# Optimization experiments

Measured on AMD Instinct MI355X. Metric: run time of the kernel, lower is better.

Reference implementation:

```python
import jax, jax.numpy as jnp
import numpy as np

D_MODEL = 1024
D_HEAD = 128


def setup_inputs() -> dict:
    key = jax.random.key(0)
    kx, kq, kk, kv, ko = jax.random.split(key, 5)
    x = jax.random.normal(kx, (4, 2048, D_MODEL), dtype=jnp.float32)
    # xavier-uniform-ish init scale
    s_in = (6.0 / (D_MODEL + D_HEAD)) ** 0.5
    wq = jax.random.uniform(kq, (D_MODEL, D_HEAD), minval=-s_in, maxval=s_in, dtype=jnp.float32)
    wk = jax.random.uniform(kk, (D_MODEL, D_HEAD), minval=-s_in, maxval=s_in, dtype=jnp.float32)
    wv = jax.random.uniform(kv, (D_MODEL, D_HEAD), minval=-s_in, maxval=s_in, dtype=jnp.float32)
    wo = jax.random.uniform(ko, (D_HEAD, D_MODEL), minval=-s_in, maxval=s_in, dtype=jnp.float32)
    return {"x": x, "wq": wq, "wk": wk, "wv": wv, "wo": wo}


def reference(x, wq, wk, wv, wo):
    # x: [b, s, d_model]
    s = x.shape[1]
    scale = 1.0 / (D_HEAD ** 0.5)
    q = jnp.einsum('bsd,dh->bsh', x, wq)
    k = jnp.einsum('bsd,dh->bsh', x, wk)
    v = jnp.einsum('bsd,dh->bsh', x, wv)
    scores = jnp.einsum('bqh,bkh->bqk', q, k) * scale  # [b, s, s]
    causal = jnp.tril(jnp.ones((s, s), dtype=bool))
    scores = jnp.where(causal, scores, -jnp.inf)
    attn = jax.nn.softmax(scores, axis=-1)
    ctx = jnp.einsum('bqk,bkh->bqh', attn, v)
    return jnp.einsum('bsh,hd->bsd', ctx, wo)
```

## Files before the change

kernel.cpp:

```cpp
#include <hip/hip_runtime.h>
#include <hip/hip_bf16.h>
#include <math.h>

typedef _Float16 half8 __attribute__((ext_vector_type(8)));
typedef _Float16 half4_t __attribute__((ext_vector_type(4)));
typedef _Float16 half2_t __attribute__((ext_vector_type(2)));
typedef float floatx4 __attribute__((ext_vector_type(4)));
typedef float floatx2 __attribute__((ext_vector_type(2)));

#define MFMA16(a, b, c) __builtin_amdgcn_mfma_f32_16x16x32_f16(a, b, c, 0, 0, 0)
#define MASKVAL (-30000.0f)
#define QSCALE 0.1275261529f

__global__ __launch_bounds__(256) void wprep(
    const float* __restrict__ wq, const float* __restrict__ wk,
    const float* __restrict__ wv, const float* __restrict__ wo,
    _Float16* __restrict__ wqt, _Float16* __restrict__ wkt,
    _Float16* __restrict__ wvt, _Float16* __restrict__ wot) {
  __shared__ float T[32][36];
  int bx = blockIdx.x, tid = threadIdx.x;
  const float* src;
  _Float16* dst;
  int R, C, r0, c0;
  float sc = 1.0f;
  if (bx < 384) {
    int p = bx >> 7, t = bx & 127;
    src = (p == 0) ? wq : (p == 1) ? wk : wv;
    dst = (p == 0) ? wqt : (p == 1) ? wkt : wvt;
    if (p == 0) sc = QSCALE;
    R = 1024; C = 128;
    r0 = (t & 31) * 32; c0 = (t >> 5) * 32;
  } else {
    int t = bx - 384;
    src = wo; dst = wot;
    R = 128; C = 1024;
    r0 = (t & 3) * 32; c0 = (t >> 2) * 32;
  }
  {
    int row = tid >> 3, c4 = (tid & 7) * 4;
    float4 f = *(const float4*)&src[(size_t)(r0 + row) * C + c0 + c4];
    T[row][c4] = f.x; T[row][c4 + 1] = f.y; T[row][c4 + 2] = f.z; T[row][c4 + 3] = f.w;
  }
  __syncthreads();
  {
    int cc = tid >> 3, r4 = (tid & 7) * 4;
    half4_t h;
    h[0] = (_Float16)(T[r4 + 0][cc] * sc);
    h[1] = (_Float16)(T[r4 + 1][cc] * sc);
    h[2] = (_Float16)(T[r4 + 2][cc] * sc);
    h[3] = (_Float16)(T[r4 + 3][cc] * sc);
    *(half4_t*)&dst[(size_t)(c0 + cc) * R + r0 + r4] = h;
  }
}

__global__ __launch_bounds__(256, 3) void qkv_gemm(
    const float* __restrict__ x, const _Float16* __restrict__ wqt,
    const _Float16* __restrict__ wkt, const _Float16* __restrict__ wvt,
    _Float16* __restrict__ Qh, _Float16* __restrict__ Kh,
    _Float16* __restrict__ Vt) {
  __shared__ _Float16 A_lds[32 * 136];
  __shared__ _Float16 B_lds[128 * 136];
  int tid = threadIdx.x;
  int w = tid >> 6, lane = tid & 63, quad = lane >> 4, l16 = lane & 15;
  int m0 = blockIdx.x * 32;
  int proj = blockIdx.y;
  const _Float16* wt = (proj == 0) ? wqt : (proj == 1) ? wkt : wvt;
  floatx4 zero = {0.f, 0.f, 0.f, 0.f};
  floatx4 acc[4];
#pragma unroll
  for (int t = 0; t < 4; t++) acc[t] = zero;

  int arow = tid >> 3, ac0 = (tid & 7) * 16;
  int brow = tid >> 1, bc0 = (tid & 1) * 64;
  int mw = (w >> 1) * 16, nw = (w & 1) * 64;

  const float* asrc = x + (size_t)(m0 + arow) * 1024 + ac0;
  const _Float16* bsrc = wt + (size_t)brow * 1024 + bc0;

  float4 af[4];
  half8 bf[8];
#pragma unroll
  for (int i = 0; i < 4; i++) af[i] = ((const float4*)asrc)[i];
#pragma unroll
  for (int i = 0; i < 8; i++) bf[i] = ((const half8*)bsrc)[i];

  for (int k0 = 0; k0 < 1024; k0 += 128) {
    {
      half8 h0, h1;
      h0[0] = (_Float16)af[0].x; h0[1] = (_Float16)af[0].y;
      h0[2] = (_Float16)af[0].z; h0[3] = (_Float16)af[0].w;
      h0[4] = (_Float16)af[1].x; h0[5] = (_Float16)af[1].y;
      h0[6] = (_Float16)af[1].z; h0[7] = (_Float16)af[1].w;
      h1[0] = (_Float16)af[2].x; h1[1] = (_Float16)af[2].y;
      h1[2] = (_Float16)af[2].z; h1[3] = (_Float16)af[2].w;
      h1[4] = (_Float16)af[3].x; h1[5] = (_Float16)af[3].y;
      h1[6] = (_Float16)af[3].z; h1[7] = (_Float16)af[3].w;
      *(half8*)&A_lds[arow * 136 + ac0] = h0;
      *(half8*)&A_lds[arow * 136 + ac0 + 8] = h1;
    }
#pragma unroll
    for (int i = 0; i < 8; i++)
      *(half8*)&B_lds[brow * 136 + bc0 + i * 8] = bf[i];
    __syncthreads();

    if (k0 + 128 < 1024) {
      const float* a2 = asrc + k0 + 128;
      const _Float16* b2 = bsrc + k0 + 128;
#pragma unroll
      for (int i = 0; i < 4; i++) af[i] = ((const float4*)a2)[i];
#pragma unroll
      for (int i = 0; i < 8; i++) bf[i] = ((const half8*)b2)[i];
    }

    half8 a[4];
#pragma unroll
    for (int c = 0; c < 4; c++)
      a[c] = *(const half8*)&A_lds[(mw + l16) * 136 + c * 32 + quad * 8];
#pragma unroll
    for (int t = 0; t < 4; t++)
#pragma unroll
      for (int c = 0; c < 4; c++) {
        half8 b = *(const half8*)&B_lds[(nw + t * 16 + l16) * 136 + c * 32 + quad * 8];
        acc[t] = MFMA16(a[c], b, acc[t]);
      }
    __syncthreads();
  }
  if (proj < 2) {
#pragma unroll
    for (int t = 0; t < 4; t++)
#pragma unroll
      for (int r = 0; r < 4; r++) {
        int row = m0 + mw + quad * 4 + r;
        int col = nw + t * 16 + l16;
        _Float16 v = (_Float16)acc[t][r];
        if (proj == 0) Qh[(size_t)row * 128 + col] = v;
        else           Kh[(size_t)row * 128 + col] = v;
      }
  } else {
    _Float16* Vl = B_lds;
#pragma unroll
    for (int t = 0; t < 4; t++)
#pragma unroll
      for (int r = 0; r < 4; r++) {
        int lrow = mw + quad * 4 + r;
        int col = nw + t * 16 + l16;
        Vl[col * 40 + lrow] = (_Float16)acc[t][r];
      }
    __syncthreads();
    int col = tid >> 1, hh = tid & 1;
    int bb = m0 >> 11, s0 = (m0 & 2047) + hh * 16;
    half8 h0 = *(half8*)&Vl[col * 40 + hh * 16];
    half8 h1 = *(half8*)&Vl[col * 40 + hh * 16 + 8];
    _Float16* dstv = Vt + ((size_t)(bb * 128 + col)) * 2048 + s0;
    *(half8*)&dstv[0] = h0;
    *(half8*)&dstv[8] = h1;
  }
}

__global__ __launch_bounds__(256, 3) void attn_partial(
    const _Float16* __restrict__ Qh, const _Float16* __restrict__ Kh,
    const _Float16* __restrict__ Vt, _Float16* __restrict__ Opart,
    float* __restrict__ Ml) {
  __shared__ _Float16 KV_lds[128 * 136];
  __shared__ _Float16 P_lds[4 * 16 * 136];
  int tid = threadIdx.x;
  int w = tid >> 6, lane = tid & 63, quad = lane >> 4, l16 = lane & 15;
  int g = (int)blockIdx.x;
  int b = g & 3;
  int r = g >> 2;
  int m = (int)sqrtf((float)r * 0.5f);
  while (2 * m * (m + 1) > r) m--;
  while (2 * (m + 1) * (m + 2) <= r) m++;
  int r0_ = r - 2 * m * (m + 1);
  int qdiv = r0_ / (m + 1);
  int qt = 4 * m + qdiv;
  int kc = r0_ - qdiv * (m + 1);
  int q0 = qt * 64, k0 = kc * 256;
  int kmax = (qt + 1) * 64;
  int len = kmax - k0; if (len > 256) len = 256;
  int nsub = (len + 127) >> 7;
  int qw0 = q0 + w * 16;
  int sidx = (b * 32 + qt) * 8 + kc;

  const _Float16* Kb = Qh;
  Kb = Kh + (size_t)b * 2048 * 128;
  const _Float16* Vb = Vt + (size_t)b * 128 * 2048;

  half8 aq[4];
  {
    const _Float16* qbase = Qh + (size_t)(b * 2048 + qw0 + l16) * 128;
#pragma unroll
    for (int c = 0; c < 4; c++) aq[c] = *(const half8*)&qbase[c * 32 + quad * 8];
  }

  int srow = tid >> 1, scol = (tid & 1) * 64;
  floatx4 zero = {0.f, 0.f, 0.f, 0.f};
  floatx4 O[8];
#pragma unroll
  for (int t = 0; t < 8; t++) O[t] = zero;
  float m_r[4] = {MASKVAL, MASKVAL, MASKVAL, MASKVAL};
  float l_r[4] = {0.f, 0.f, 0.f, 0.f};

  for (int s = 0; s < nsub; s++) {
    int ks = k0 + s * 128;
    if (s) __syncthreads();
#pragma unroll
    for (int i = 0; i < 8; i++)
      *(half8*)&KV_lds[srow * 136 + scol + i * 8] =
          *(const half8*)&Kb[(size_t)(ks + srow) * 128 + scol + i * 8];
    half8 vreg[8];
#pragma unroll
    for (int i = 0; i < 8; i++)
      vreg[i] = *(const half8*)&Vb[(size_t)srow * 2048 + ks + scol + i * 8];
    __syncthreads();

    floatx4 sa[8];
#pragma unroll
    for (int t = 0; t < 8; t++) sa[t] = zero;
#pragma unroll
    for (int t = 0; t < 8; t++)
#pragma unroll
      for (int c = 0; c < 4; c++) {
        half8 bk = *(const half8*)&KV_lds[(t * 16 + l16) * 136 + c * 32 + quad * 8];
        sa[t] = MFMA16(aq[c], bk, sa[t]);
      }

    float sc[4];
#pragma unroll
    for (int j = 0; j < 4; j++) {
      int query = qw0 + quad * 4 + j;
      float mx = MASKVAL;
#pragma unroll
      for (int t = 0; t < 8; t++) {
        float v = (ks + t * 16 + l16 > query) ? MASKVAL : sa[t][j];
        sa[t][j] = v;
        mx = fmaxf(mx, v);
      }
#pragma unroll
      for (int off = 1; off < 16; off <<= 1) mx = fmaxf(mx, __shfl_xor(mx, off));
      float mnew = fmaxf(m_r[j], mx);
      float scj = exp2f(m_r[j] - mnew);
      float rs = 0.f;
#pragma unroll
      for (int t = 0; t < 8; t++) {
        float e = exp2f(sa[t][j] - mnew);
        sa[t][j] = e;
        rs += e;
      }
#pragma unroll
      for (int off = 1; off < 16; off <<= 1) rs += __shfl_xor(rs, off);
      l_r[j] = l_r[j] * scj + rs;
      m_r[j] = mnew;
      sc[j] = scj;
    }
#pragma unroll
    for (int t = 0; t < 8; t++)
#pragma unroll
      for (int j = 0; j < 4; j++) O[t][j] *= sc[j];

    __syncthreads();
#pragma unroll
    for (int i = 0; i < 8; i++)
      *(half8*)&KV_lds[srow * 136 + scol + i * 8] = vreg[i];
    _Float16* P = P_lds + w * 16 * 136;
#pragma unroll
    for (int j = 0; j < 4; j++)
#pragma unroll
      for (int t = 0; t < 8; t++)
        P[(quad * 4 + j) * 136 + t * 16 + l16] = (_Float16)sa[t][j];
    __syncthreads();

#pragma unroll
    for (int c2 = 0; c2 < 4; c2++) {
      half8 ap = *(const half8*)&P[l16 * 136 + c2 * 32 + quad * 8];
#pragma unroll
      for (int t = 0; t < 8; t++) {
        half8 bv = *(const half8*)&KV_lds[(t * 16 + l16) * 136 + c2 * 32 + quad * 8];
        O[t] = MFMA16(ap, bv, O[t]);
      }
    }
  }

  size_t obase = (size_t)sidx * 8192;
#pragma unroll
  for (int t = 0; t < 8; t++)
#pragma unroll
    for (int j = 0; j < 4; j++)
      Opart[obase + (size_t)(w * 16 + quad * 4 + j) * 128 + t * 16 + l16] = (_Float16)O[t][j];
  if (l16 == 0)
#pragma unroll
    for (int j = 0; j < 4; j++) {
      int row = w * 16 + quad * 4 + j;
      floatx2 ml;
      ml[0] = m_r[j];
      ml[1] = l_r[j];
      *(floatx2*)&Ml[(size_t)sidx * 128 + row * 2] = ml;
    }
}

__global__ __launch_bounds__(256) void attn_combine(
    const _Float16* __restrict__ Opart, const float* __restrict__ Ml,
    _Float16* __restrict__ ctx) {
  int tid = threadIdx.x;
  int w = tid >> 6, lane = tid & 63;
  int row = blockIdx.x * 4 + w;
  int b = row >> 11, s = row & 2047;
  int qt = s >> 6, ri = s & 63;
  int nkc = (qt + 4) >> 2;
  int sidx0 = (b * 32 + qt) * 8;
  float mv[8], lv[8];
#pragma unroll
  for (int i = 0; i < 8; i++) {
    if (i < nkc) {
      floatx2 ml = *(const floatx2*)&Ml[(size_t)(sidx0 + i) * 128 + ri * 2];
      mv[i] = ml[0]; lv[i] = ml[1];
    } else { mv[i] = MASKVAL; lv[i] = 0.f; }
  }
  float M = MASKVAL;
#pragma unroll
  for (int i = 0; i < 8; i++) M = fmaxf(M, mv[i]);
  float L = 0.f, a0 = 0.f, a1 = 0.f;
#pragma unroll
  for (int i = 0; i < 8; i++) {
    if (i < nkc) {
      float scv = exp2f(mv[i] - M);
      L += lv[i] * scv;
      half2_t o = *(const half2_t*)&Opart[(size_t)(sidx0 + i) * 8192 + (size_t)ri * 128 + lane * 2];
      a0 += scv * (float)o[0];
      a1 += scv * (float)o[1];
    }
  }
  float inv = 1.f / L;
  half2_t hv;
  hv[0] = (_Float16)(a0 * inv);
  hv[1] = (_Float16)(a1 * inv);
  *(half2_t*)&ctx[(size_t)row * 128 + lane * 2] = hv;
}

__global__ __launch_bounds__(256) void out_gemm(
    const _Float16* __restrict__ ctx, const _Float16* __restrict__ wot,
    float* __restrict__ out) {
  __shared__ _Float16 A_lds[64 * 136];
  __shared__ _Float16 B_lds[128 * 136];
  int tid = threadIdx.x;
  int w = tid >> 6, lane = tid & 63, quad = lane >> 4, l16 = lane & 15;
  int m0 = blockIdx.x * 64, n0 = blockIdx.y * 128;
  {
    int row = tid >> 2, kk = (tid & 3) * 32;
#pragma unroll
    for (int i = 0; i < 4; i++)
      *(half8*)&A_lds[row * 136 + kk + i * 8] =
          *(const half8*)&ctx[(size_t)(m0 + row) * 128 + kk + i * 8];
  }
  {
    int n = tid >> 1, kk = (tid & 1) * 64;
#pragma unroll
    for (int i = 0; i < 8; i++)
      *(half8*)&B_lds[n * 136 + kk + i * 8] =
          *(const half8*)&wot[(size_t)(n0 + n) * 128 + kk + i * 8];
  }
  __syncthreads();
  floatx4 zero = {0.f, 0.f, 0.f, 0.f};
  floatx4 acc[8];
#pragma unroll
  for (int t = 0; t < 8; t++) acc[t] = zero;
  half8 a[4];
#pragma unroll
  for (int c = 0; c < 4; c++) a[c] = *(const half8*)&A_lds[(w * 16 + l16) * 136 + c * 32 + quad * 8];
#pragma unroll
  for (int t = 0; t < 8; t++)
#pragma unroll
    for (int c = 0; c < 4; c++) {
      half8 b = *(const half8*)&B_lds[(t * 16 + l16) * 136 + c * 32 + quad * 8];
      acc[t] = MFMA16(a[c], b, acc[t]);
    }
#pragma unroll
  for (int t = 0; t < 8; t++)
#pragma unroll
    for (int r = 0; r < 4; r++) {
      int row = m0 + w * 16 + quad * 4 + r;
      out[(size_t)row * 1024 + n0 + t * 16 + l16] = acc[t][r];
    }
}

extern "C" void kernel_launch(void* const* d_in, const int* in_sizes, int n_in,
                              void* d_out, int out_size, void* d_ws, size_t ws_size,
                              hipStream_t stream) {
  const float* x = (const float*)d_in[0];
  const float* wq = (const float*)d_in[1];
  const float* wk = (const float*)d_in[2];
  const float* wv = (const float*)d_in[3];
  const float* wo = (const float*)d_in[4];
  char* ws = (char*)d_ws;
  _Float16* wqt = (_Float16*)(ws + 0);
  _Float16* wkt = (_Float16*)(ws + 262144);
  _Float16* wvt = (_Float16*)(ws + 524288);
  _Float16* wot = (_Float16*)(ws + 786432);
  _Float16* Qh  = (_Float16*)(ws + 1048576);
  _Float16* Kh  = (_Float16*)(ws + 3145728);
  _Float16* Vt  = (_Float16*)(ws + 5242880);
  _Float16* ctxh = (_Float16*)(ws + 7340032);
  _Float16* Opart = (_Float16*)(ws + 9437184);
  float* Ml = (float*)(ws + 26214400);
  float* out = (float*)d_out;

  wprep<<<512, 256, 0, stream>>>(wq, wk, wv, wo, wqt, wkt, wvt, wot);
  qkv_gemm<<<dim3(256, 3), 256, 0, stream>>>(x, wqt, wkt, wvt, Qh, Kh, Vt);
  attn_partial<<<576, 256, 0, stream>>>(Qh, Kh, Vt, Opart, Ml);
  attn_combine<<<2048, 256, 0, stream>>>(Opart, Ml, ctxh);
  out_gemm<<<dim3(128, 8), 256, 0, stream>>>(ctxh, wot, out);
}
```

Measured before the change: 156.8 us.

## Fuse attention combine into output projection and retile QKV GEMM warps

The separate split-K combine kernel and output GEMM are merged into one kernel. Each block combines 32 query rows into LDS and then loops over all eight 128-column chunks of Wo, double-buffering the Wo tile through registers. This drops one launch and the fp16 ctx round trip through global memory, but shrinks the grid to 256 blocks that each serialize eight N-chunks. The QKV GEMM warp tiling also changes from 16x64 to 32x32 per warp, so each B fragment loaded from LDS feeds two MFMAs.

```diff
diff --git a/kernel.cpp b/kernel.cpp
--- a/kernel.cpp
+++ b/kernel.cpp
@@ -66,13 +66,15 @@
   int proj = blockIdx.y;
   const _Float16* wt = (proj == 0) ? wqt : (proj == 1) ? wkt : wvt;
   floatx4 zero = {0.f, 0.f, 0.f, 0.f};
-  floatx4 acc[4];
-#pragma unroll
-  for (int t = 0; t < 4; t++) acc[t] = zero;
+  floatx4 acc[2][2];
+#pragma unroll
+  for (int mi = 0; mi < 2; mi++)
+#pragma unroll
+    for (int ni = 0; ni < 2; ni++) acc[mi][ni] = zero;
 
   int arow = tid >> 3, ac0 = (tid & 7) * 16;
   int brow = tid >> 1, bc0 = (tid & 1) * 64;
-  int mw = (w >> 1) * 16, nw = (w & 1) * 64;
+  int nw = w * 32;
 
   const float* asrc = x + (size_t)(m0 + arow) * 1024 + ac0;
   const _Float16* bsrc = wt + (size_t)brow * 1024 + bc0;
@@ -112,40 +114,47 @@
       for (int i = 0; i < 8; i++) bf[i] = ((const half8*)b2)[i];
     }
 
-    half8 a[4];
-#pragma unroll
-    for (int c = 0; c < 4; c++)
-      a[c] = *(const half8*)&A_lds[(mw + l16) * 136 + c * 32 + quad * 8];
-#pragma unroll
-    for (int t = 0; t < 4; t++)
+    half8 a[2][4];
+#pragma unroll
+    for (int c = 0; c < 4; c++) {
+      a[0][c] = *(const half8*)&A_lds[l16 * 136 + c * 32 + quad * 8];
+      a[1][c] = *(const half8*)&A_lds[(16 + l16) * 136 + c * 32 + quad * 8];
+    }
+#pragma unroll
+    for (int ni = 0; ni < 2; ni++)
 #pragma unroll
       for (int c = 0; c < 4; c++) {
-        half8 b = *(const half8*)&B_lds[(nw + t * 16 + l16) * 136 + c * 32 + quad * 8];
-        acc[t] = MFMA16(a[c], b, acc[t]);
+        half8 b = *(const half8*)&B_lds[(nw + ni * 16 + l16) * 136 + c * 32 + quad * 8];
+        acc[0][ni] = MFMA16(a[0][c], b, acc[0][ni]);
+        acc[1][ni] = MFMA16(a[1][c], b, acc[1][ni]);
       }
     __syncthreads();
   }
   if (proj < 2) {
 #pragma unroll
-    for (int t = 0; t < 4; t++)
-#pragma unroll
-      for (int r = 0; r < 4; r++) {
-        int row = m0 + mw + quad * 4 + r;
-        int col = nw + t * 16 + l16;
-        _Float16 v = (_Float16)acc[t][r];
-        if (proj == 0) Qh[(size_t)row * 128 + col] = v;
-        else           Kh[(size_t)row * 128 + col] = v;
-      }
+    for (int mi = 0; mi < 2; mi++)
+#pragma unroll
+      for (int ni = 0; ni < 2; ni++)
+#pragma unroll
+        for (int r = 0; r < 4; r++) {
+          int row = m0 + mi * 16 + quad * 4 + r;
+          int col = nw + ni * 16 + l16;
+          _Float16 v = (_Float16)acc[mi][ni][r];
+          if (proj == 0) Qh[(size_t)row * 128 + col] = v;
+          else           Kh[(size_t)row * 128 + col] = v;
+        }
   } else {
     _Float16* Vl = B_lds;
 #pragma unroll
-    for (int t = 0; t < 4; t++)
-#pragma unroll
-      for (int r = 0; r < 4; r++) {
-        int lrow = mw + quad * 4 + r;
-        int col = nw + t * 16 + l16;
-        Vl[col * 40 + lrow] = (_Float16)acc[t][r];
-      }
+    for (int mi = 0; mi < 2; mi++)
+#pragma unroll
+      for (int ni = 0; ni < 2; ni++)
+#pragma unroll
+        for (int r = 0; r < 4; r++) {
+          int lrow = mi * 16 + quad * 4 + r;
+          int col = nw + ni * 16 + l16;
+          Vl[col * 40 + lrow] = (_Float16)acc[mi][ni][r];
+        }
     __syncthreads();
     int col = tid >> 1, hh = tid & 1;
     int bb = m0 >> 11, s0 = (m0 & 2047) + hh * 16;
@@ -182,8 +191,7 @@
   int qw0 = q0 + w * 16;
   int sidx = (b * 32 + qt) * 8 + kc;
 
-  const _Float16* Kb = Qh;
-  Kb = Kh + (size_t)b * 2048 * 128;
+  const _Float16* Kb = Kh + (size_t)b * 2048 * 128;
   const _Float16* Vb = Vt + (size_t)b * 128 * 2048;
 
   half8 aq[4];
@@ -298,89 +306,112 @@
     }
 }
 
-__global__ __launch_bounds__(256) void attn_combine(
+__global__ __launch_bounds__(256) void combine_out(
     const _Float16* __restrict__ Opart, const float* __restrict__ Ml,
-    _Float16* __restrict__ ctx) {
+    const _Float16* __restrict__ wot, float* __restrict__ out) {
+  __shared__ _Float16 A_lds[32 * 136];
+  __shared__ _Float16 B_lds[128 * 136];
   int tid = threadIdx.x;
-  int w = tid >> 6, lane = tid & 63;
-  int row = blockIdx.x * 4 + w;
-  int b = row >> 11, s = row & 2047;
-  int qt = s >> 6, ri = s & 63;
+  int r0 = blockIdx.x * 32;
+  int b = r0 >> 11, s0 = r0 & 2047;
+  int qt = s0 >> 6, rbase = s0 & 63;
   int nkc = (qt + 4) >> 2;
   int sidx0 = (b * 32 + qt) * 8;
-  float mv[8], lv[8];
-#pragma unroll
-  for (int i = 0; i < 8; i++) {
-    if (i < nkc) {
-      floatx2 ml = *(const floatx2*)&Ml[(size_t)(sidx0 + i) * 128 + ri * 2];
-      mv[i] = ml[0]; lv[i] = ml[1];
-    } else { mv[i] = MASKVAL; lv[i] = 0.f; }
-  }
-  float M = MASKVAL;
-#pragma unroll
-  for (int i = 0; i < 8; i++) M = fmaxf(M, mv[i]);
-  float L = 0.f, a0 = 0.f, a1 = 0.f;
-#pragma unroll
-  for (int i = 0; i < 8; i++) {
-    if (i < nkc) {
-      float scv = exp2f(mv[i] - M);
-      L += lv[i] * scv;
-      half2_t o = *(const half2_t*)&Opart[(size_t)(sidx0 + i) * 8192 + (size_t)ri * 128 + lane * 2];
-      a0 += scv * (float)o[0];
-      a1 += scv * (float)o[1];
-    }
-  }
-  float inv = 1.f / L;
-  half2_t hv;
-  hv[0] = (_Float16)(a0 * inv);
-  hv[1] = (_Float16)(a1 * inv);
-  *(half2_t*)&ctx[(size_t)row * 128 + lane * 2] = hv;
-}
-
-__global__ __launch_bounds__(256) void out_gemm(
-    const _Float16* __restrict__ ctx, const _Float16* __restrict__ wot,
-    float* __restrict__ out) {
-  __shared__ _Float16 A_lds[64 * 136];
-  __shared__ _Float16 B_lds[128 * 136];
-  int tid = threadIdx.x;
+
+  {
+    int lr = tid >> 3, c0 = (tid & 7) * 16;
+    int ri = rbase + lr;
+    float mv[8], lv[8];
+#pragma unroll
+    for (int i = 0; i < 8; i++) {
+      if (i < nkc) {
+        floatx2 ml = *(const floatx2*)&Ml[(size_t)(sidx0 + i) * 128 + ri * 2];
+        mv[i] = ml[0]; lv[i] = ml[1];
+      } else { mv[i] = MASKVAL; lv[i] = 0.f; }
+    }
+    float M = MASKVAL;
+#pragma unroll
+    for (int i = 0; i < 8; i++) M = fmaxf(M, mv[i]);
+    float L = 0.f;
+    float a0[16];
+#pragma unroll
+    for (int c = 0; c < 16; c++) a0[c] = 0.f;
+#pragma unroll
+    for (int i = 0; i < 8; i++) {
+      if (i < nkc) {
+        float scv = exp2f(mv[i] - M);
+        L += lv[i] * scv;
+        const _Float16* op = &Opart[(size_t)(sidx0 + i) * 8192 + (size_t)ri * 128 + c0];
+        half8 o0 = *(const half8*)&op[0];
+        half8 o1 = *(const half8*)&op[8];
+#pragma unroll
+        for (int c = 0; c < 8; c++) {
+          a0[c]     += scv * (float)o0[c];
+          a0[8 + c] += scv * (float)o1[c];
+        }
+      }
+    }
+    float inv = 1.f / L;
+    half8 h0, h1;
+#pragma unroll
+    for (int c = 0; c < 8; c++) {
+      h0[c] = (_Float16)(a0[c] * inv);
+      h1[c] = (_Float16)(a0[8 + c] * inv);
+    }
+    *(half8*)&A_lds[lr * 136 + c0] = h0;
+    *(half8*)&A_lds[lr * 136 + c0 + 8] = h1;
+  }
+
   int w = tid >> 6, lane = tid & 63, quad = lane >> 4, l16 = lane & 15;
-  int m0 = blockIdx.x * 64, n0 = blockIdx.y * 128;
-  {
-    int row = tid >> 2, kk = (tid & 3) * 32;
-#pragma unroll
-    for (int i = 0; i < 4; i++)
-      *(half8*)&A_lds[row * 136 + kk + i * 8] =
-          *(const half8*)&ctx[(size_t)(m0 + row) * 128 + kk + i * 8];
-  }
-  {
-    int n = tid >> 1, kk = (tid & 1) * 64;
+  int bn = tid >> 1, bk = (tid & 1) * 64;
+  half8 bf[8];
+#pragma unroll
+  for (int i = 0; i < 8; i++)
+    bf[i] = *(const half8*)&wot[(size_t)bn * 128 + bk + i * 8];
+  __syncthreads();
+
+  half8 a[2][4];
+#pragma unroll
+  for (int c = 0; c < 4; c++) {
+    a[0][c] = *(const half8*)&A_lds[l16 * 136 + c * 32 + quad * 8];
+    a[1][c] = *(const half8*)&A_lds[(16 + l16) * 136 + c * 32 + quad * 8];
+  }
+  floatx4 zero = {0.f, 0.f, 0.f, 0.f};
+  for (int nc = 0; nc < 8; nc++) {
 #pragma unroll
     for (int i = 0; i < 8; i++)
-      *(half8*)&B_lds[n * 136 + kk + i * 8] =
-          *(const half8*)&wot[(size_t)(n0 + n) * 128 + kk + i * 8];
-  }
-  __syncthreads();
-  floatx4 zero = {0.f, 0.f, 0.f, 0.f};
-  floatx4 acc[8];
-#pragma unroll
-  for (int t = 0; t < 8; t++) acc[t] = zero;
-  half8 a[4];
-#pragma unroll
-  for (int c = 0; c < 4; c++) a[c] = *(const half8*)&A_lds[(w * 16 + l16) * 136 + c * 32 + quad * 8];
-#pragma unroll
-  for (int t = 0; t < 8; t++)
-#pragma unroll
-    for (int c = 0; c < 4; c++) {
-      half8 b = *(const half8*)&B_lds[(t * 16 + l16) * 136 + c * 32 + quad * 8];
-      acc[t] = MFMA16(a[c], b, acc[t]);
-    }
-#pragma unroll
-  for (int t = 0; t < 8; t++)
-#pragma unroll
-    for (int r = 0; r < 4; r++) {
-      int row = m0 + w * 16 + quad * 4 + r;
-      out[(size_t)row * 1024 + n0 + t * 16 + l16] = acc[t][r];
-    }
+      *(half8*)&B_lds[bn * 136 + bk + i * 8] = bf[i];
+    __syncthreads();
+    if (nc < 7) {
+#pragma unroll
+      for (int i = 0; i < 8; i++)
+        bf[i] = *(const half8*)&wot[(size_t)((nc + 1) * 128 + bn) * 128 + bk + i * 8];
+    }
+    floatx4 acc[2][2];
+#pragma unroll
+    for (int mi = 0; mi < 2; mi++)
+#pragma unroll
+      for (int ni = 0; ni < 2; ni++) acc[mi][ni] = zero;
+    int nw = w * 32;
+#pragma unroll
+    for (int ni = 0; ni < 2; ni++)
+#pragma unroll
+      for (int c = 0; c < 4; c++) {
+        half8 bb = *(const half8*)&B_lds[(nw + ni * 16 + l16) * 136 + c * 32 + quad * 8];
+        acc[0][ni] = MFMA16(a[0][c], bb, acc[0][ni]);
+        acc[1][ni] = MFMA16(a[1][c], bb, acc[1][ni]);
+      }
+#pragma unroll
+    for (int mi = 0; mi < 2; mi++)
+#pragma unroll
+      for (int ni = 0; ni < 2; ni++)
+#pragma unroll
+        for (int r = 0; r < 4; r++) {
+          int row = r0 + mi * 16 + quad * 4 + r;
+          out[(size_t)row * 1024 + nc * 128 + nw + ni * 16 + l16] = acc[mi][ni][r];
+        }
+    __syncthreads();
+  }
 }
 
 extern "C" void kernel_launch(void* const* d_in, const int* in_sizes, int n_in,
@@ -399,7 +430,6 @@
   _Float16* Qh  = (_Float16*)(ws + 1048576);
   _Float16* Kh  = (_Float16*)(ws + 3145728);
   _Float16* Vt  = (_Float16*)(ws + 5242880);
-  _Float16* ctxh = (_Float16*)(ws + 7340032);
   _Float16* Opart = (_Float16*)(ws + 9437184);
   float* Ml = (float*)(ws + 26214400);
   float* out = (float*)d_out;
@@ -407,6 +437,5 @@
   wprep<<<512, 256, 0, stream>>>(wq, wk, wv, wo, wqt, wkt, wvt, wot);
   qkv_gemm<<<dim3(256, 3), 256, 0, stream>>>(x, wqt, wkt, wvt, Qh, Kh, Vt);
   attn_partial<<<576, 256, 0, stream>>>(Qh, Kh, Vt, Opart, Ml);
-  attn_combine<<<2048, 256, 0, stream>>>(Opart, Ml, ctxh);
-  out_gemm<<<dim3(128, 8), 256, 0, stream>>>(ctxh, wot, out);
+  combine_out<<<256, 256, 0, stream>>>(Opart, Ml, wot, out);
 }
```

Measured after the change: 157.2 us. Within noise of the previous version (+0.2%).
